# Optimization experiments

Hardware: AMD Instinct MI355X
Metric: run time of the kernel (lower is better)

## Reference

```python
import jax, jax.numpy as jnp
import numpy as np

N = 20000; E = 320000; G = 64; C_IN = 128; H = 128; L = 3; S = 4
EPS = 1e-5; SLOPE = 0.01  # GraphNorm eps, leaky_relu negative slope


def _kruskal(ei, ew, n):
    # Kruskal MST over edges sorted by usage-count weight; returns bidirectional MST edges
    # and the updated usage counts (used edges get +1), mirroring kruskal_mst_track_usage.
    order = np.argsort(ew, kind='stable')
    s = ei[0][order]; d = ei[1][order]
    parent = np.arange(n)
    def find(u):
        while parent[u] != u:
            parent[u] = parent[parent[u]]
            u = parent[u]
        return u
    mst = []; used = []
    for i in range(s.shape[0]):
        ru = find(s[i]); rv = find(d[i])
        if ru != rv:
            parent[ru] = rv
            mst.append((s[i], d[i]))
            used.append(order[i])
            if len(mst) == n - 1:
                break
    ew = ew.copy(); ew[np.asarray(used)] += 1
    m = np.asarray(mst, dtype=np.int64).T  # [2, ~n-1]
    return np.concatenate([m, m[::-1]], axis=1), ew  # bidirectional


def setup_inputs():
    rng = np.random.default_rng(0)
    x = rng.standard_normal((N, C_IN), dtype=np.float32)
    edge_index = rng.integers(0, N, size=(2, E)).astype(np.int64)
    batch = np.sort(rng.integers(0, G, size=N)).astype(np.int64)
    # split_graph: shuffle edges, then repeatedly extract MSTs (no_grad / CPU in original)
    perm = rng.permutation(E)
    ei_p = edge_index[:, perm]
    ew = np.zeros(E, dtype=np.int64)
    msts = []
    for _ in range(S - 1):  # only splits 0..3 are used; split 0 is the shuffled full graph
        m, ew = _kruskal(ei_p, ew, N)
        msts.append(m)
    def gp(shape):
        return jnp.asarray((0.05 * rng.standard_normal(shape)).astype(np.float32))
    return {
        'x': jnp.asarray(x),
        'emb_W': gp((C_IN, H)), 'emb_b': gp((H,)),
        'main_W': gp((L, H, H)), 'main_b': gp((L, H)),
        'main_gw': jnp.ones((L, H), jnp.float32), 'main_gb': jnp.zeros((L, H), jnp.float32), 'main_gms': jnp.ones((L, H), jnp.float32),
        'loc_W': gp((L, H, H)), 'loc_b': gp((L, H)),
        'loc_gw': jnp.ones((L, H), jnp.float32), 'loc_gb': jnp.zeros((L, H), jnp.float32), 'loc_gms': jnp.ones((L, H), jnp.float32),
        'merge_W': gp((H * (S + 1), H)), 'merge_b': gp((H,)),
        'edge_index': jnp.asarray(edge_index),
        'edges0': jnp.asarray(ei_p),
        'edges1': jnp.asarray(msts[0]),
        'edges2': jnp.asarray(msts[1]),
        'edges3': jnp.asarray(msts[2]),
        'batch': jnp.asarray(batch),
    }


def _seg(v, idx, n):
    return jax.ops.segment_sum(v, idx, num_segments=n)


def _gcn(x, W, b, src, dst):
    # PyG GCNConv with self-loops and symmetric normalization
    n = x.shape[0]
    h = x @ W
    deg = _seg(jnp.ones(src.shape[0], x.dtype), dst, n) + 1.0
    dinv = jax.lax.rsqrt(deg)
    coef = (dinv[src] * dinv[dst])[:, None]
    out = _seg(h[src] * coef, dst, n) + h * (dinv * dinv)[:, None]  # neighbors + self-loop
    return out + b


def _graph_norm(x, batch, cnt, w, b, ms):
    # PyG GraphNorm: per-graph mean with learnable mean_scale, per-graph variance
    mean = _seg(x, batch, G) / cnt
    out = x - ms * mean[batch]
    var = _seg(out * out, batch, G) / cnt
    inv = jax.lax.rsqrt(var + EPS)
    return w * out * inv[batch] + b


def _gnn(x, src, dst, Ws, bs, gw, gb, gms, batch, cnt):
    hist = []
    for l in range(L):
        x = _gcn(x, Ws[l], bs[l], src, dst)
        x = _graph_norm(x, batch, cnt, gw[l], gb[l], gms[l])
        x = jax.nn.leaky_relu(x, SLOPE)
        hist.append(x)  # dropout in eval mode = identity
    return hist


def _forward(x, emb_W, emb_b, main_W, main_b, main_gw, main_gb, main_gms,
             loc_W, loc_b, loc_gw, loc_gb, loc_gms, merge_W, merge_b,
             edge_index, edges0, edges1, edges2, edges3, batch):
    cnt = jnp.maximum(_seg(jnp.ones(N, x.dtype), batch, G), 1.0)[:, None]  # [G,1]
    h = x @ emb_W + emb_b
    main_hist = _gnn(h, edge_index[0], edge_index[1], main_W, main_b, main_gw, main_gb, main_gms, batch, cnt)
    split_hists = [_gnn(h, e[0], e[1], loc_W, loc_b, loc_gw, loc_gb, loc_gms, batch, cnt)
                   for e in (edges0, edges1, edges2, edges3)]
    gs = []
    for l in range(L):
        xl = jnp.concatenate([sh[l] for sh in split_hists] + [main_hist[l]], axis=1)  # [N, 5H]
        xl = xl @ merge_W + merge_b
        gs.append(_seg(xl, batch, G) / cnt)  # global_mean_pool
    return jnp.mean(jnp.stack(gs), axis=0)  # [G, H]


def reference(x, emb_W, emb_b, main_W, main_b, main_gw, main_gb, main_gms,
              loc_W, loc_b, loc_gw, loc_gb, loc_gms, merge_W, merge_b,
              edge_index, edges0, edges1, edges2, edges3, batch):
    return _forward(x, emb_W, emb_b, main_W, main_b, main_gw, main_gb, main_gms,
                    loc_W, loc_b, loc_gw, loc_gb, loc_gms, merge_W, merge_b,
                    edge_index, edges0, edges1, edges2, edges3, batch)
```

## Files before the change

### kernel.cpp

```cpp
#include <hip/hip_runtime.h>

#define NN 20000
#define NNP 20032
#define NH 128
#define NG 64
#define NLAY 3
#define NCH 5
#define GEPS 1e-5f
#define GSLOPE 0.01f

typedef unsigned short u16;
typedef unsigned int u32;
typedef __attribute__((ext_vector_type(8))) short short8;
typedef __attribute__((ext_vector_type(4))) float float4v;
typedef __attribute__((ext_vector_type(2))) float f32x2;

__device__ __forceinline__ u16 f2bf(float f) {
  union { float f; u32 u; } v; v.f = f;
  u32 r = (v.u + 0x7fffu + ((v.u >> 16) & 1u)) >> 16;
  return (u16)r;
}

struct ZP {
  const u16* A[NCH];
  const u16* W[NCH];
  u16* Y[NCH];
  int ystride[NCH];
  u16* Xo[NCH];
  const float* bias[NCH];
  const float* gw[NCH];
  const float* gb[NCH];
  const float* gms[NCH];
  const float* pgw[NCH];
  const float* pgb[NCH];
  int colbase[NCH];
};

struct ES4 {
  const int* e[4];
  int cnt[4];
  int off[4];
};


__global__ __launch_bounds__(1024) void k_scan(const int* __restrict__ deg,
                                               int* __restrict__ indptr,
                                               int* __restrict__ cursor,
                                               float* __restrict__ dinv,
                                               const int* __restrict__ batch,
                                               int* __restrict__ counts,
                                               int* __restrict__ gstart) {
  int s = blockIdx.x;
  int t = threadIdx.x;
  if (s == 4) {
    int g = t;
    if (g < NG) {
      auto lb = [&](int key) {
        int lo = 0, hi = NN;
        while (lo < hi) {
          int mid = (lo + hi) >> 1;
          if (batch[mid] < key) lo = mid + 1; else hi = mid;
        }
        return lo;
      };
      int a = lb(g), b = lb(g + 1);
      gstart[g] = a;
      counts[g] = b - a;
    }
    return;
  }
  const int* d = deg + s * NN;
  int* ip = indptr + s * (NN + 1);
  int* cu = cursor + s * (NN + 1);
  int lane = t & 63, wv = t >> 6;
  __shared__ int wsum[16];
  int run = 0;
  const int NT = (NN + 1023) / 1024;
  for (int tile = 0; tile < NT; tile++) {
    int idx = tile * 1024 + t;
    int v = 0;
    if (idx < NN) {
      v = d[idx];
      dinv[s * NN + idx] = rsqrtf((float)v + 1.0f);
    }
    int x = v;
#pragma unroll
    for (int o = 1; o < 64; o <<= 1) {
      int y = __shfl_up(x, o);
      if (lane >= o) x += y;
    }
    if (lane == 63) wsum[wv] = x;
    __syncthreads();
    if (wv == 0) {
      int y = (lane < 16) ? wsum[lane] : 0;
#pragma unroll
      for (int o = 1; o < 16; o <<= 1) {
        int z = __shfl_up(y, o);
        if (lane >= o) y += z;
      }
      if (lane < 16) wsum[lane] = y;
    }
    __syncthreads();
    int waveoff = (wv == 0) ? 0 : wsum[wv - 1];
    int excl = run + waveoff + x - v;
    if (idx < NN) { ip[idx] = excl; cu[idx] = excl; }
    run += wsum[15];
    __syncthreads();
  }
  if (t == 0) { ip[NN] = run; cu[NN] = run; }
}

__global__ void k_fill(ES4 es, const float* __restrict__ dinv, int* __restrict__ cursor,
                       u32* __restrict__ ent) {
  int s = blockIdx.y;
  int i = blockIdx.x * 256 + threadIdx.x;
  int E = es.cnt[s];
  if (i >= E) return;
  int src = es.e[s][i];
  int dst = es.e[s][E + i];
  int pos = atomicAdd(&cursor[s * (NN + 1) + dst], 1);
  float c = dinv[s * NN + src] * dinv[s * NN + dst];
  ent[es.off[s] + pos] = (u32)src | ((u32)f2bf(c) << 16);
}

__global__ __launch_bounds__(256) void k_setup(ES4 es, int* __restrict__ deg,
                                               const float* __restrict__ embW,
                                               const float* __restrict__ locW,
                                               const float* __restrict__ mainW,
                                               u16* __restrict__ wt) {
  int ybk = blockIdx.y;
  if (ybk < 4) {
    int s = ybk;
    int i = blockIdx.x * 256 + threadIdx.x;
    int E = es.cnt[s];
    if (i < E) atomicAdd(&deg[s * NN + es.e[s][E + i]], 1);
    return;
  }
  if (blockIdx.x >= 16) return;
  int mat = ybk - 4;
  const float* W = (mat == 0) ? embW : ((mat <= 3) ? locW + (mat - 1) * NH * NH
                                                   : mainW + (mat - 4) * NH * NH);
  int tile = blockIdx.x;
  int tk = (tile >> 2) * 32;
  int tn = (tile & 3) * 32;
  __shared__ float tl[32][33];
  int c = threadIdx.x & 31, r = threadIdx.x >> 5;
#pragma unroll
  for (int rr = 0; rr < 32; rr += 8)
    tl[r + rr][c] = W[(size_t)(tk + r + rr) * NH + tn + c];
  __syncthreads();
#pragma unroll
  for (int rr = 0; rr < 32; rr += 8)
    wt[(size_t)mat * NH * NH + (size_t)(tn + r + rr) * NH + tk + c] = f2bf(tl[c][r + rr]);
}


__global__ __launch_bounds__(256) void k_gemm0(const float* __restrict__ x,
                                               const u16* __restrict__ wt,
                                               const float* __restrict__ embb,
                                               u16* __restrict__ ydual) {
  __shared__ u16 As[64][136];
  __shared__ u16 Bs[128][136];
  int t = threadIdx.x;
  int row0 = blockIdx.x * 64;
  int c = t & 15, rs = t >> 4;
#pragma unroll
  for (int pass = 0; pass < 4; pass++) {
    int r = pass * 16 + rs;
    int gr = row0 + r;
    uint4 o = make_uint4(0, 0, 0, 0);
    if (gr < NN) {
      float4 a = *(const float4*)(x + (size_t)gr * NH + c * 8);
      float4 b = *(const float4*)(x + (size_t)gr * NH + c * 8 + 4);
      o.x = f2bf(a.x) | ((u32)f2bf(a.y) << 16);
      o.y = f2bf(a.z) | ((u32)f2bf(a.w) << 16);
      o.z = f2bf(b.x) | ((u32)f2bf(b.y) << 16);
      o.w = f2bf(b.z) | ((u32)f2bf(b.w) << 16);
    }
    *(uint4*)(&As[r][c * 8]) = o;
  }
#pragma unroll
  for (int pass = 0; pass < 8; pass++) {
    int n = pass * 16 + rs;
    *(uint4*)(&Bs[n][c * 8]) = *(const uint4*)(wt + (size_t)n * NH + c * 8);
  }
  __syncthreads();
  int lane = t & 63, w = t >> 6;
  int m16 = lane & 15, quad = lane >> 4;
  float4v acc[8];
#pragma unroll
  for (int i = 0; i < 8; i++) acc[i] = (float4v)(0.f);
#pragma unroll
  for (int kk = 0; kk < 4; kk++) {
    short8 av = *(const short8*)(&As[w * 16 + m16][kk * 32 + quad * 8]);
#pragma unroll
    for (int ct = 0; ct < 8; ct++) {
      short8 bv = *(const short8*)(&Bs[ct * 16 + m16][kk * 32 + quad * 8]);
      acc[ct] = __builtin_amdgcn_mfma_f32_16x16x32_bf16(av, bv, acc[ct], 0, 0, 0);
    }
  }
  __syncthreads();
#pragma unroll
  for (int ct = 0; ct < 8; ct++) {
    float bv = embb[ct * 16 + m16];
#pragma unroll
    for (int r = 0; r < 4; r++)
      As[w * 16 + quad * 4 + r][ct * 16 + m16] = f2bf(acc[ct][r] + bv);
  }
  {
    const u16* wl = wt + (size_t)1 * NH * NH;
#pragma unroll
    for (int pass = 0; pass < 8; pass++) {
      int n = pass * 16 + rs;
      *(uint4*)(&Bs[n][c * 8]) = *(const uint4*)(wl + (size_t)n * NH + c * 8);
    }
  }
  __syncthreads();
  float4v acc0[8];
#pragma unroll
  for (int i = 0; i < 8; i++) acc0[i] = (float4v)(0.f);
#pragma unroll
  for (int kk = 0; kk < 4; kk++) {
    short8 av = *(const short8*)(&As[w * 16 + m16][kk * 32 + quad * 8]);
#pragma unroll
    for (int ct = 0; ct < 8; ct++) {
      short8 bv = *(const short8*)(&Bs[ct * 16 + m16][kk * 32 + quad * 8]);
      acc0[ct] = __builtin_amdgcn_mfma_f32_16x16x32_bf16(av, bv, acc0[ct], 0, 0, 0);
    }
  }
  __syncthreads();
  {
    const u16* wm = wt + (size_t)4 * NH * NH;
#pragma unroll
    for (int pass = 0; pass < 8; pass++) {
      int n = pass * 16 + rs;
      *(uint4*)(&Bs[n][c * 8]) = *(const uint4*)(wm + (size_t)n * NH + c * 8);
    }
  }
  __syncthreads();
  float4v acc4[8];
#pragma unroll
  for (int i = 0; i < 8; i++) acc4[i] = (float4v)(0.f);
#pragma unroll
  for (int kk = 0; kk < 4; kk++) {
    short8 av = *(const short8*)(&As[w * 16 + m16][kk * 32 + quad * 8]);
#pragma unroll
    for (int ct = 0; ct < 8; ct++) {
      short8 bv = *(const short8*)(&Bs[ct * 16 + m16][kk * 32 + quad * 8]);
      acc4[ct] = __builtin_amdgcn_mfma_f32_16x16x32_bf16(av, bv, acc4[ct], 0, 0, 0);
    }
  }
  __syncthreads();
#pragma unroll
  for (int ct = 0; ct < 8; ct++) {
#pragma unroll
    for (int r = 0; r < 4; r++) {
      As[w * 16 + quad * 4 + r][ct * 16 + m16] = f2bf(acc0[ct][r]);
      Bs[w * 16 + quad * 4 + r][ct * 16 + m16] = f2bf(acc4[ct][r]);
    }
  }
  __syncthreads();
#pragma unroll
  for (int pass = 0; pass < 4; pass++) {
    int r = pass * 16 + rs;
    int gr = row0 + r;
    if (gr < NN) {
      *(uint4*)(ydual + (size_t)gr * 256 + c * 8) = *(const uint4*)(&As[r][c * 8]);
      *(uint4*)(ydual + (size_t)gr * 256 + 128 + c * 8) = *(const uint4*)(&Bs[r][c * 8]);
    }
  }
}

__global__ __launch_bounds__(256) void k_gemm_bf(ZP p, const int* __restrict__ batch,
                                                 const float* __restrict__ aff) {
  int zi = blockIdx.y;
  const u16* __restrict__ X = p.A[zi];
  const u16* __restrict__ Wt = p.W[zi];
  u16* __restrict__ Y = p.Y[zi];
  const float* __restrict__ gw = p.pgw[zi];
  const float* __restrict__ gb = p.pgb[zi];
  int yst = p.ystride[zi];
  __shared__ u16 As[64][136];
  __shared__ u16 Bs[128][136];
  int t = threadIdx.x;
  int row0 = blockIdx.x * 64;
  int c = t & 15, rs = t >> 4;
  float4 wA = *(const float4*)(gw + c * 8);
  float4 wB = *(const float4*)(gw + c * 8 + 4);
  float4 bA = *(const float4*)(gb + c * 8);
  float4 bB = *(const float4*)(gb + c * 8 + 4);
  float wv8[8] = {wA.x, wA.y, wA.z, wA.w, wB.x, wB.y, wB.z, wB.w};
  float bv8[8] = {bA.x, bA.y, bA.z, bA.w, bB.x, bB.y, bB.z, bB.w};
#pragma unroll
  for (int pass = 0; pass < 4; pass++) {
    int r = pass * 16 + rs;
    int gr = row0 + r;
    int grc = (gr < NN) ? gr : (NN - 1);
    int gg = batch[grc];
    const float* ab = aff + ((size_t)zi * NG + gg) * 2 * NH;
    uint4 xv = *(const uint4*)(X + (size_t)grc * NH + c * 8);
    float4 mA = *(const float4*)(ab + c * 8);
    float4 mB = *(const float4*)(ab + c * 8 + 4);
    float4 iA = *(const float4*)(ab + NH + c * 8);
    float4 iB = *(const float4*)(ab + NH + c * 8 + 4);
    float mm[8] = {mA.x, mA.y, mA.z, mA.w, mB.x, mB.y, mB.z, mB.w};
    float iv[8] = {iA.x, iA.y, iA.z, iA.w, iB.x, iB.y, iB.z, iB.w};
    u32 xw[4] = {xv.x, xv.y, xv.z, xv.w};
    uint4 ou;
    u32* op = (u32*)&ou;
#pragma unroll
    for (int j = 0; j < 4; j++) {
      float v0 = __uint_as_float(xw[j] << 16);
      float v1 = __uint_as_float(xw[j] & 0xffff0000u);
      float o0 = wv8[2 * j] * (v0 - mm[2 * j]) * iv[2 * j] + bv8[2 * j];
      float o1 = wv8[2 * j + 1] * (v1 - mm[2 * j + 1]) * iv[2 * j + 1] + bv8[2 * j + 1];
      o0 = (o0 >= 0.f) ? o0 : GSLOPE * o0;
      o1 = (o1 >= 0.f) ? o1 : GSLOPE * o1;
      op[j] = (u32)f2bf(o0) | ((u32)f2bf(o1) << 16);
    }
    *(uint4*)(&As[r][c * 8]) = ou;
  }
#pragma unroll
  for (int pass = 0; pass < 8; pass++) {
    int n = pass * 16 + rs;
    *(uint4*)(&Bs[n][c * 8]) = *(const uint4*)(Wt + (size_t)n * NH + c * 8);
  }
  __syncthreads();
  int lane = t & 63, w = t >> 6;
  int m16 = lane & 15, quad = lane >> 4;
  float4v acc[8];
#pragma unroll
  for (int i = 0; i < 8; i++) acc[i] = (float4v)(0.f);
#pragma unroll
  for (int kk = 0; kk < 4; kk++) {
    short8 av = *(const short8*)(&As[w * 16 + m16][kk * 32 + quad * 8]);
#pragma unroll
    for (int ct = 0; ct < 8; ct++) {
      short8 bv = *(const short8*)(&Bs[ct * 16 + m16][kk * 32 + quad * 8]);
      acc[ct] = __builtin_amdgcn_mfma_f32_16x16x32_bf16(av, bv, acc[ct], 0, 0, 0);
    }
  }
  __syncthreads();
#pragma unroll
  for (int ct = 0; ct < 8; ct++) {
#pragma unroll
    for (int r = 0; r < 4; r++) {
      As[w * 16 + quad * 4 + r][ct * 16 + m16] = f2bf(acc[ct][r]);
    }
  }
  __syncthreads();
#pragma unroll
  for (int pass = 0; pass < 4; pass++) {
    int r = pass * 16 + rs;
    int gr = row0 + r;
    if (gr < NN) *(uint4*)(Y + (size_t)gr * yst + c * 8) = *(const uint4*)(&As[r][c * 8]);
  }
}

__device__ __forceinline__ f32x2 bf2x2(u32 v) {
  f32x2 r;
  r.x = __uint_as_float(v << 16);
  r.y = __uint_as_float(v & 0xffff0000u);
  return r;
}

__device__ __forceinline__ void fma8p(f32x2* a, uint4 v, float cf) {
  f32x2 c2; c2.x = cf; c2.y = cf;
  a[0] += c2 * bf2x2(v.x);
  a[1] += c2 * bf2x2(v.y);
  a[2] += c2 * bf2x2(v.z);
  a[3] += c2 * bf2x2(v.w);
}

__device__ __forceinline__ void fin_chain(const float* a, const u16* Yb, int st, int node,
                                          int fo, float d2, const float* bias,
                                          u16* __restrict__ Xo) {
  uint4 sv = *(const uint4*)(Yb + (size_t)node * st + fo);
  float s[8] = {
    __uint_as_float(sv.x << 16), __uint_as_float(sv.x & 0xffff0000u),
    __uint_as_float(sv.y << 16), __uint_as_float(sv.y & 0xffff0000u),
    __uint_as_float(sv.z << 16), __uint_as_float(sv.z & 0xffff0000u),
    __uint_as_float(sv.w << 16), __uint_as_float(sv.w & 0xffff0000u)};
  float4 b0 = *(const float4*)(bias + fo);
  float4 b1 = *(const float4*)(bias + fo + 4);
  float bb[8] = {b0.x, b0.y, b0.z, b0.w, b1.x, b1.y, b1.z, b1.w};
  float o[8];
#pragma unroll
  for (int j = 0; j < 8; j++) o[j] = a[j] + d2 * s[j] + bb[j];
  uint4 ou;
  u32* op = (u32*)&ou;
#pragma unroll
  for (int j = 0; j < 4; j++)
    op[j] = (u32)f2bf(o[2 * j]) | ((u32)f2bf(o[2 * j + 1]) << 16);
  *(uint4*)(Xo + (size_t)node * NH + fo) = ou;
}

__global__ __launch_bounds__(256) void k_agg2(ZP p, const int* __restrict__ indptr,
                                              const u32* __restrict__ ent,
                                              const float* __restrict__ dinv, int4 entoff) {
  int b = blockIdx.x;
  int wv = threadIdx.x >> 6, lane = threadIdx.x & 63;
  int g = lane >> 4;
  int fo = (lane & 15) * 8;
  if (b < 5000) {
    int node = b * 4 + wv;
    int beg = indptr[node], end = indptr[node + 1];
    const u16* __restrict__ Y0 = p.Y[0];
    const u16* __restrict__ Y4 = p.Y[4];
    int st = p.ystride[0];
    f32x2 a0[4], a4[4];
#pragma unroll
    for (int j = 0; j < 4; j++) { a0[j] = (f32x2)(0.f); a4[j] = (f32x2)(0.f); }
    int e = beg + g;
    for (; e + 4 < end; e += 8) {
      u32 sa = ent[e];
      u32 sb = ent[e + 4];
      size_t ra = (size_t)(sa & 0xffffu) * st + fo;
      size_t rb = (size_t)(sb & 0xffffu) * st + fo;
      uint4 va0 = *(const uint4*)(Y0 + ra);
      uint4 va4 = *(const uint4*)(Y4 + ra);
      uint4 vb0 = *(const uint4*)(Y0 + rb);
      uint4 vb4 = *(const uint4*)(Y4 + rb);
      float ca = __uint_as_float(sa & 0xffff0000u);
      float cb = __uint_as_float(sb & 0xffff0000u);
      fma8p(a0, va0, ca); fma8p(a4, va4, ca);
      fma8p(a0, vb0, cb); fma8p(a4, vb4, cb);
    }
    if (e < end) {
      u32 sc = ent[e];
      float cf = __uint_as_float(sc & 0xffff0000u);
      size_t ro = (size_t)(sc & 0xffffu) * st + fo;
      uint4 v0 = *(const uint4*)(Y0 + ro);
      uint4 v4 = *(const uint4*)(Y4 + ro);
      fma8p(a0, v0, cf);
      fma8p(a4, v4, cf);
    }
    float* f0 = (float*)a0;
    float* f4 = (float*)a4;
#pragma unroll
    for (int j = 0; j < 8; j++) {
      f0[j] += __shfl_xor(f0[j], 16);
      f0[j] += __shfl_xor(f0[j], 32);
      f4[j] += __shfl_xor(f4[j], 16);
      f4[j] += __shfl_xor(f4[j], 32);
    }
    if (g == 0) {
      float di = dinv[node];
      float d2 = di * di;
      fin_chain(f0, Y0, st, node, fo, d2, p.bias[0], p.Xo[0]);
      fin_chain(f4, Y4, st, node, fo, d2, p.bias[4], p.Xo[4]);
    }
  } else {
    int mb = b - 5000;
    int s = 1 + mb / 1250;
    int node = (mb % 1250) * 16 + wv * 4 + g;
    const int* ip = indptr + s * (NN + 1);
    int eb = (s == 1) ? entoff.y : ((s == 2) ? entoff.z : entoff.w);
    const u16* __restrict__ Y = p.Y[s];
    int st = p.ystride[s];
    int beg = ip[node], end = ip[node + 1];
    const u32* __restrict__ ev = ent + eb;
    f32x2 a[4];
#pragma unroll
    for (int j = 0; j < 4; j++) a[j] = (f32x2)(0.f);
    int e = beg;
    for (; e + 1 < end; e += 2) {
      u32 s0 = ev[e];
      u32 s1 = ev[e + 1];
      uint4 v0 = *(const uint4*)(Y + (size_t)(s0 & 0xffffu) * st + fo);
      uint4 v1 = *(const uint4*)(Y + (size_t)(s1 & 0xffffu) * st + fo);
      fma8p(a, v0, __uint_as_float(s0 & 0xffff0000u));
      fma8p(a, v1, __uint_as_float(s1 & 0xffff0000u));
    }
    if (e < end) {
      u32 sc = ev[e];
      uint4 v = *(const uint4*)(Y + (size_t)(sc & 0xffffu) * st + fo);
      fma8p(a, v, __uint_as_float(sc & 0xffff0000u));
    }
    float di = dinv[s * NN + node];
    float d2 = di * di;
    fin_chain((float*)a, Y, st, node, fo, d2, p.bias[s], p.Xo[s]);
  }
}

__global__ __launch_bounds__(256) void k_norm2(ZP p, const int* __restrict__ gstart,
                                               const int* __restrict__ counts,
                                               float* __restrict__ Ml,
                                               float* __restrict__ aff) {
  int g = blockIdx.x, zi = blockIdx.y, fc = blockIdx.z;
  const u16* __restrict__ X = p.Xo[zi];
  int t = threadIdx.x;
  int fj = t & 15;
  int f2 = fc * 32 + fj * 2;
  int rh = t >> 4;
  int start = gstart[g], cnt = counts[g];
  __shared__ float red[4][16][17];
  float s0 = 0.f, s1 = 0.f, q0 = 0.f, q1 = 0.f;
  for (int i = rh; i < cnt; i += 16) {
    u32 v = *(const u32*)(X + (size_t)(start + i) * NH + f2);
    float v0 = __uint_as_float(v << 16), v1 = __uint_as_float(v & 0xffff0000u);
    s0 += v0; q0 += v0 * v0;
    s1 += v1; q1 += v1 * v1;
  }
  red[0][rh][fj] = s0; red[1][rh][fj] = s1;
  red[2][rh][fj] = q0; red[3][rh][fj] = q1;
  __syncthreads();
#pragma unroll
  for (int off = 8; off >= 1; off >>= 1) {
    if (rh < off) {
      red[0][rh][fj] += red[0][rh + off][fj];
      red[1][rh][fj] += red[1][rh + off][fj];
      red[2][rh][fj] += red[2][rh + off][fj];
      red[3][rh][fj] += red[3][rh + off][fj];
    }
    __syncthreads();
  }
  float cntf = fmaxf((float)cnt, 1.f);
  float w0 = p.gw[zi][f2], w1 = p.gw[zi][f2 + 1];
  float b0 = p.gb[zi][f2], b1 = p.gb[zi][f2 + 1];
  float ms0 = p.gms[zi][f2], ms1 = p.gms[zi][f2 + 1];
  float mean0 = red[0][0][fj] / cntf, mean1 = red[1][0][fj] / cntf;
  float mm0 = ms0 * mean0, mm1 = ms1 * mean1;
  float var0 = red[2][0][fj] / cntf - (2.f * ms0 - ms0 * ms0) * mean0 * mean0;
  float var1 = red[3][0][fj] / cntf - (2.f * ms1 - ms1 * ms1) * mean1 * mean1;
  float inv0 = rsqrtf(var0 + GEPS), inv1 = rsqrtf(var1 + GEPS);
  __syncthreads();
  float m0 = 0.f, m1 = 0.f;
  for (int i = rh; i < cnt; i += 16) {
    size_t ro = (size_t)(start + i) * NH + f2;
    u32 v = *(const u32*)(X + ro);
    float v0 = __uint_as_float(v << 16), v1 = __uint_as_float(v & 0xffff0000u);
    float o0 = w0 * (v0 - mm0) * inv0 + b0;
    float o1 = w1 * (v1 - mm1) * inv1 + b1;
    o0 = (o0 >= 0.f) ? o0 : GSLOPE * o0;
    o1 = (o1 >= 0.f) ? o1 : GSLOPE * o1;
    m0 += o0; m1 += o1;
  }
  red[0][rh][fj] = m0; red[1][rh][fj] = m1;
  __syncthreads();
#pragma unroll
  for (int off = 8; off >= 1; off >>= 1) {
    if (rh < off) {
      red[0][rh][fj] += red[0][rh + off][fj];
      red[1][rh][fj] += red[1][rh + off][fj];
    }
    __syncthreads();
  }
  if (rh == 0) {
    int col = p.colbase[zi] + f2;
    Ml[(size_t)g * 640 + col] = red[0][0][fj];
    Ml[(size_t)g * 640 + col + 1] = red[1][0][fj];
    if (aff) {
      float* ab = aff + ((size_t)zi * NG + g) * 2 * NH;
      ab[f2] = mm0; ab[f2 + 1] = mm1;
      ab[NH + f2] = inv0; ab[NH + f2 + 1] = inv1;
    }
  }
}

__global__ __launch_bounds__(256) void k_mergeout(const float* __restrict__ M,
                                                  const float* __restrict__ mergeW,
                                                  const float* __restrict__ mergeb,
                                                  const int* __restrict__ counts,
                                                  float* __restrict__ out) {
  int g = blockIdx.x;
  int f = threadIdx.x & 127, h = threadIdx.x >> 7;
  __shared__ float mrow[640];
  __shared__ float red[128];
  float acc = 0.f;
  for (int l = 0; l < NLAY; l++) {
    const float* Mr = M + ((size_t)l * NG + g) * 640;
    for (int i = threadIdx.x; i < 640; i += 256) mrow[i] = Mr[i];
    __syncthreads();
    float s = 0.f;
    int k0 = h * 320;
#pragma unroll 8
    for (int k = k0; k < k0 + 320; k++) s += mrow[k] * mergeW[(size_t)k * NH + f];
    if (h) red[f] = s;
    __syncthreads();
    if (!h) acc += s + red[f];
    __syncthreads();
  }
  if (!h) {
    float cnt = fmaxf((float)counts[g], 1.f);
    out[(size_t)g * NH + f] = acc / (3.f * cnt) + mergeb[f];
  }
}


struct Offs {
  size_t counts, gstart, deg, M, dinv, indptr, cursor, ent, wt, ydual, aff;
  size_t yb[NCH], xo[NCH];
  size_t memset1_off, memset1_len, total;
};

static size_t build_offs(Offs& o, int Etot) {
  size_t off = 0;
  auto alloc = [&](size_t bytes) -> size_t {
    off = (off + 255) & ~(size_t)255;
    size_t s = off;
    off += bytes;
    return s;
  };
  o.counts = alloc(NG * 4);
  o.gstart = alloc(NG * 4);
  o.deg = alloc((size_t)4 * NN * 4);
  o.memset1_off = o.deg;
  o.memset1_len = (size_t)4 * NN * 4;
  o.M = alloc((size_t)NLAY * NG * 640 * 4);
  o.dinv = alloc((size_t)4 * NN * 4);
  o.indptr = alloc((size_t)4 * (NN + 1) * 4);
  o.cursor = alloc((size_t)4 * (NN + 1) * 4);
  o.ent = alloc((size_t)Etot * 4);
  o.wt = alloc((size_t)7 * NH * NH * 2);
  o.aff = alloc((size_t)NCH * NG * 2 * NH * 4);
  o.ydual = alloc((size_t)NN * 256 * 2);
  for (int i = 1; i < 4; i++) o.yb[i] = alloc((size_t)NN * NH * 2);
  for (int i = 0; i < NCH; i++) {
    o.xo[i] = alloc((size_t)NNP * NH * 2);
  }
  o.total = off;
  return off;
}

extern "C" void kernel_launch(void* const* d_in, const int* in_sizes, int n_in,
                              void* d_out, int out_size, void* d_ws, size_t ws_size,
                              hipStream_t stream) {
  if (n_in < 21) return;
  const float* x = (const float*)d_in[0];
  const float* embW = (const float*)d_in[1];
  const float* embb = (const float*)d_in[2];
  const float* mainW = (const float*)d_in[3];
  const float* mainb = (const float*)d_in[4];
  const float* maingw = (const float*)d_in[5];
  const float* maingb = (const float*)d_in[6];
  const float* maingms = (const float*)d_in[7];
  const float* locW = (const float*)d_in[8];
  const float* locb = (const float*)d_in[9];
  const float* locgw = (const float*)d_in[10];
  const float* locgb = (const float*)d_in[11];
  const float* locgms = (const float*)d_in[12];
  const float* mergeW = (const float*)d_in[13];
  const float* mergeb = (const float*)d_in[14];
  const int* edge_index = (const int*)d_in[15];
  const int* edges1 = (const int*)d_in[17];
  const int* edges2 = (const int*)d_in[18];
  const int* edges3 = (const int*)d_in[19];
  const int* batch = (const int*)d_in[20];

  int E0 = in_sizes[15] / 2;
  int E1 = in_sizes[17] / 2, E2 = in_sizes[18] / 2, E3 = in_sizes[19] / 2;
  int Etot = E0 + E1 + E2 + E3;
  int maxE = E0 > E1 ? E0 : E1;
  maxE = maxE > E2 ? maxE : E2;
  maxE = maxE > E3 ? maxE : E3;

  Offs o;
  if (build_offs(o, Etot) > ws_size) return;

  char* ws = (char*)d_ws;
  int* counts = (int*)(ws + o.counts);
  int* gstart = (int*)(ws + o.gstart);
  int* deg = (int*)(ws + o.deg);
  float* M = (float*)(ws + o.M);
  float* dinv = (float*)(ws + o.dinv);
  int* indptr = (int*)(ws + o.indptr);
  int* cursor = (int*)(ws + o.cursor);
  u32* ent = (u32*)(ws + o.ent);
  u16* wt = (u16*)(ws + o.wt);
  float* aff = (float*)(ws + o.aff);
  u16* ydual = (u16*)(ws + o.ydual);
  u16 *yb[NCH], *xo[NCH];
  for (int i = 1; i < 4; i++) yb[i] = (u16*)(ws + o.yb[i]);
  for (int i = 0; i < NCH; i++) xo[i] = (u16*)(ws + o.xo[i]);

  ES4 es;
  es.e[0] = edge_index; es.e[1] = edges1; es.e[2] = edges2; es.e[3] = edges3;
  es.cnt[0] = E0; es.cnt[1] = E1; es.cnt[2] = E2; es.cnt[3] = E3;
  es.off[0] = 0; es.off[1] = E0; es.off[2] = E0 + E1; es.off[3] = E0 + E1 + E2;
  int4 entoff = make_int4(0, E0, E0 + E1, E0 + E1 + E2);

  hipMemsetAsync(ws + o.memset1_off, 0, o.memset1_len, stream);
  k_setup<<<dim3((maxE + 255) / 256, 11), 256, 0, stream>>>(es, deg, embW, locW, mainW, wt);
  k_scan<<<5, 1024, 0, stream>>>(deg, indptr, cursor, dinv, batch, counts, gstart);
  k_fill<<<dim3((maxE + 255) / 256, 4), 256, 0, stream>>>(es, dinv, cursor, ent);

  const int nrb = (NN + 63) / 64;

  k_gemm0<<<nrb, 256, 0, stream>>>(x, wt, embb, ydual);

  for (int l = 0; l < NLAY; l++) {
    int lp = (l > 0) ? (l - 1) : 0;
    ZP p = {};
    for (int zi = 0; zi < NCH; zi++) {
      bool isMain = (zi == 4);
      p.A[zi] = (const u16*)xo[zi];
      p.W[zi] = wt + (size_t)((isMain ? 4 : 1) + l) * NH * NH;
      if (zi == 0) { p.Y[0] = ydual; p.ystride[0] = 256; }
      else if (zi == 4) { p.Y[4] = ydual + 128; p.ystride[4] = 256; }
      else { p.Y[zi] = yb[zi]; p.ystride[zi] = 128; }
      p.Xo[zi] = xo[zi];
      p.bias[zi] = (isMain ? mainb : locb) + (size_t)l * NH;
      p.gw[zi] = (isMain ? maingw : locgw) + (size_t)l * NH;
      p.gb[zi] = (isMain ? maingb : locgb) + (size_t)l * NH;
      p.gms[zi] = (isMain ? maingms : locgms) + (size_t)l * NH;
      p.pgw[zi] = (isMain ? maingw : locgw) + (size_t)lp * NH;
      p.pgb[zi] = (isMain ? maingb : locgb) + (size_t)lp * NH;
      p.colbase[zi] = isMain ? 512 : zi * NH;
    }
    if (l == 0) {
      p.Y[1] = ydual; p.Y[2] = ydual; p.Y[3] = ydual;
      p.ystride[1] = p.ystride[2] = p.ystride[3] = 256;
    } else {
      k_gemm_bf<<<dim3(nrb, NCH), 256, 0, stream>>>(p, batch, aff);
    }
    k_agg2<<<8750, 256, 0, stream>>>(p, indptr, ent, dinv, entoff);
    k_norm2<<<dim3(NG, NCH, 4), 256, 0, stream>>>(p, gstart, counts,
                                                  M + (size_t)l * NG * 640,
                                                  (l == NLAY - 1) ? nullptr : aff);
  }

  k_mergeout<<<NG, 256, 0, stream>>>(M, mergeW, mergeb, counts, (float*)d_out);
}
```

Baseline: 376.3 us.

## Split full-graph aggregation across feature chunks with 16 edge lanes per node

The full-graph part of the aggregation kernel now splits each node's 128 features into four 32-wide chunks, each handled by its own block. Inside a wave, 16 edge groups of 4 lanes each walk the neighbour list, replacing 4 groups of 16 lanes, which gives more memory-level parallelism on high-degree nodes. The cost is a longer cross-lane reduction (four shuffle stages instead of two), 4x more blocks, narrower 64-byte row segments per gather, and repeated reads of the indptr and edge list per chunk. The grid grows from 8750 to 23750 blocks, and the block-to-node mapping interleaves chunks so that neighbouring blocks share node rows.

```diff
diff --git a/kernel.cpp b/kernel.cpp
--- a/kernel.cpp
+++ b/kernel.cpp
@@ -400,10 +400,12 @@
                                               const float* __restrict__ dinv, int4 entoff) {
   int b = blockIdx.x;
   int wv = threadIdx.x >> 6, lane = threadIdx.x & 63;
-  int g = lane >> 4;
-  int fo = (lane & 15) * 8;
-  if (b < 5000) {
-    int node = b * 4 + wv;
+  if (b < 20000) {
+    int chunk = (b >> 1) & 3;
+    int ng = ((b >> 3) << 1) | (b & 1);
+    int node = ng * 4 + wv;
+    int eg = lane >> 2;
+    int fo = chunk * 32 + (lane & 3) * 8;
     int beg = indptr[node], end = indptr[node + 1];
     const u16* __restrict__ Y0 = p.Y[0];
     const u16* __restrict__ Y4 = p.Y[4];
@@ -411,27 +413,12 @@
     f32x2 a0[4], a4[4];
 #pragma unroll
     for (int j = 0; j < 4; j++) { a0[j] = (f32x2)(0.f); a4[j] = (f32x2)(0.f); }
-    int e = beg + g;
-    for (; e + 4 < end; e += 8) {
-      u32 sa = ent[e];
-      u32 sb = ent[e + 4];
-      size_t ra = (size_t)(sa & 0xffffu) * st + fo;
-      size_t rb = (size_t)(sb & 0xffffu) * st + fo;
-      uint4 va0 = *(const uint4*)(Y0 + ra);
-      uint4 va4 = *(const uint4*)(Y4 + ra);
-      uint4 vb0 = *(const uint4*)(Y0 + rb);
-      uint4 vb4 = *(const uint4*)(Y4 + rb);
-      float ca = __uint_as_float(sa & 0xffff0000u);
-      float cb = __uint_as_float(sb & 0xffff0000u);
-      fma8p(a0, va0, ca); fma8p(a4, va4, ca);
-      fma8p(a0, vb0, cb); fma8p(a4, vb4, cb);
-    }
-    if (e < end) {
-      u32 sc = ent[e];
-      float cf = __uint_as_float(sc & 0xffff0000u);
-      size_t ro = (size_t)(sc & 0xffffu) * st + fo;
+    for (int e = beg + eg; e < end; e += 16) {
+      u32 s = ent[e];
+      size_t ro = (size_t)(s & 0xffffu) * st + fo;
       uint4 v0 = *(const uint4*)(Y0 + ro);
       uint4 v4 = *(const uint4*)(Y4 + ro);
+      float cf = __uint_as_float(s & 0xffff0000u);
       fma8p(a0, v0, cf);
       fma8p(a4, v4, cf);
     }
@@ -439,20 +426,26 @@
     float* f4 = (float*)a4;
 #pragma unroll
     for (int j = 0; j < 8; j++) {
+      f0[j] += __shfl_xor(f0[j], 4);
+      f4[j] += __shfl_xor(f4[j], 4);
+      f0[j] += __shfl_xor(f0[j], 8);
+      f4[j] += __shfl_xor(f4[j], 8);
       f0[j] += __shfl_xor(f0[j], 16);
+      f4[j] += __shfl_xor(f4[j], 16);
       f0[j] += __shfl_xor(f0[j], 32);
-      f4[j] += __shfl_xor(f4[j], 16);
       f4[j] += __shfl_xor(f4[j], 32);
     }
-    if (g == 0) {
+    if (eg == 0) {
       float di = dinv[node];
       float d2 = di * di;
       fin_chain(f0, Y0, st, node, fo, d2, p.bias[0], p.Xo[0]);
       fin_chain(f4, Y4, st, node, fo, d2, p.bias[4], p.Xo[4]);
     }
   } else {
-    int mb = b - 5000;
+    int mb = b - 20000;
     int s = 1 + mb / 1250;
+    int g = lane >> 4;
+    int fo = (lane & 15) * 8;
     int node = (mb % 1250) * 16 + wv * 4 + g;
     const int* ip = indptr + s * (NN + 1);
     int eb = (s == 1) ? entoff.y : ((s == 2) ? entoff.z : entoff.w);
@@ -714,7 +707,7 @@
     } else {
       k_gemm_bf<<<dim3(nrb, NCH), 256, 0, stream>>>(p, batch, aff);
     }
-    k_agg2<<<8750, 256, 0, stream>>>(p, indptr, ent, dinv, entoff);
+    k_agg2<<<23750, 256, 0, stream>>>(p, indptr, ent, dinv, entoff);
     k_norm2<<<dim3(NG, NCH, 4), 256, 0, stream>>>(p, gstart, counts,
                                                   M + (size_t)l * NG * 640,
                                                   (l == NLAY - 1) ? nullptr : aff);
```

After: 472.1 us. 25.5% more time.
